# Performance work log

Measured on AMD Instinct MI355X. Metric: run time of the kernel, lower is better.

## Reference

```python
import jax, jax.numpy as jnp
import numpy as np

# ---- module config (matches init_kwargs) ----
TEMPORAL_DIM = 64
INPUT_DIM = 3
NUM_LEVELS = 16
LEVEL_DIM = 2          # C: output channels per level
BASE_RES = 16
LOG2_HASH = 17
DESIRED_RES = 2048
ALIGN_CORNERS = False
PER_LEVEL_SCALE = float(np.exp2(np.log2(DESIRED_RES / BASE_RES) / (NUM_LEVELS - 1)))
S = float(np.log2(PER_LEVEL_SCALE))
GRID_CH = LEVEL_DIM + TEMPORAL_DIM  # channels stored per table row
PRIMES = (1, 2654435761, 805459861)  # InstantNGP fast_hash primes
B = 262144


def _level_params():
    """Static per-level (offset, hashmap_size, resolution, scale) per InstantNGP."""
    params = []
    offset = 0
    max_params = 2 ** LOG2_HASH
    for l in range(NUM_LEVELS):
        scale = float(np.exp2(l * S)) * BASE_RES - 1.0
        resolution = int(np.ceil(scale)) + 1
        res_eff = resolution if ALIGN_CORNERS else resolution + 1
        n = min(max_params, res_eff ** INPUT_DIM)
        n = int(np.ceil(n / 8) * 8)
        params.append((offset, n, resolution, scale))
        offset += n
    return params, offset

LEVELS, TABLE_ROWS = _level_params()


def setup_inputs() -> dict:
    key = jax.random.key(0)
    k1, k2, k3, k4 = jax.random.split(key, 4)
    inputs = jax.random.uniform(k1, (B, INPUT_DIM), dtype=jnp.float32)  # coords in [0,1)
    embeddings = jax.random.uniform(k2, (TABLE_ROWS, GRID_CH), dtype=jnp.float32,
                                    minval=-1e-4, maxval=1e-4)
    # temporal sliding-window rows: per sample/channel, blend two adjacent channels
    idx_a = jax.random.randint(k3, (B, LEVEL_DIM), 0, GRID_CH)
    idx_b = (idx_a + 1) % GRID_CH
    t = jax.random.uniform(k4, (B, LEVEL_DIM), dtype=jnp.float32)
    tri = jnp.stack([1.0 - t, idx_a.astype(jnp.float32), t, idx_b.astype(jnp.float32)],
                    axis=2).reshape(B, 4 * LEVEL_DIM)
    return {"inputs": inputs, "temporal_row_index": tri, "embeddings": embeddings}


def _encode(inputs, temporal_row_index, embeddings):
    n = inputs.shape[0]
    w_a = temporal_row_index[:, 0::4]                       # [B, C]
    idx_a = temporal_row_index[:, 1::4].astype(jnp.int32)   # [B, C]
    w_b = temporal_row_index[:, 2::4]
    idx_b = temporal_row_index[:, 3::4].astype(jnp.int32)
    emb_flat = embeddings.reshape(-1)
    outs = []
    for (offset, hsize, resolution, scale) in LEVELS:
        res_eff = resolution if ALIGN_CORNERS else resolution + 1
        use_hash = (res_eff ** INPUT_DIM) > hsize  # static per level
        pos = inputs * scale + (0.0 if ALIGN_CORNERS else 0.5)  # [B, D]
        pos_floor = jnp.floor(pos)
        frac = pos - pos_floor
        pos_g = pos_floor.astype(jnp.uint32)
        acc = jnp.zeros((n, LEVEL_DIM), embeddings.dtype)
        for corner in range(2 ** INPUT_DIM):
            offs = [(corner >> d) & 1 for d in range(INPUT_DIM)]
            cpos = pos_g + jnp.asarray(offs, dtype=jnp.uint32)  # [B, D]
            w = jnp.ones((n,), inputs.dtype)
            for d in range(INPUT_DIM):
                w = w * (frac[:, d] if offs[d] else 1.0 - frac[:, d])
            if use_hash:
                idx = jnp.zeros((n,), jnp.uint32)
                for d in range(INPUT_DIM):
                    idx = idx ^ (cpos[:, d] * jnp.uint32(PRIMES[d]))  # uint32 wrap
            else:
                idx = jnp.zeros((n,), jnp.uint32)
                stride = 1
                for d in range(INPUT_DIM):
                    idx = idx + cpos[:, d] * jnp.uint32(stride)
                    stride *= res_eff
            row = (idx % jnp.uint32(hsize)).astype(jnp.int32) + offset  # [B]
            base = row[:, None] * GRID_CH
            va = emb_flat[base + idx_a]  # [B, C] temporal channel A
            vb = emb_flat[base + idx_b]  # [B, C] temporal channel B
            acc = acc + w[:, None] * (w_a * va + w_b * vb)
        outs.append(acc)
    # == outputs.permute(1,0,2).reshape(B, L*C)
    return jnp.concatenate(outs, axis=1)


def reference(inputs, temporal_row_index, embeddings):
    return _encode(inputs, temporal_row_index, embeddings)
```

## Files before the change

### kernel.cpp

```cpp
#include <hip/hip_runtime.h>
#include <cmath>

#define NUM_LEVELS 16
#define GRID_CH 66
#define BLOCK 256
#define NGRP 8
#define NSL 14

typedef float float4n __attribute__((ext_vector_type(4)));
typedef float float2n __attribute__((ext_vector_type(2)));

struct LevelP { int offset; int res_eff; int use_hash; int hsize; float scale; };
struct SlP {
    int   offset[NSL];
    int   res_eff[NSL];
    int   use_hash[NSL];
    int   ssz[NSL];
    float scale[NSL];
};

static LevelP g_levels[NUM_LEVELS];
static bool init_levels() {
    long long off = 0;
    const double S = std::log2(2048.0 / 16.0) / 15.0;
    for (int l = 0; l < NUM_LEVELS; ++l) {
        double scale = std::exp2((double)l * S) * 16.0 - 1.0;
        int resolution = (int)std::ceil(scale) + 1;
        int res_eff = resolution + 1;
        long long cube = (long long)res_eff * res_eff * res_eff;
        long long n = cube < 131072 ? cube : 131072;
        n = ((n + 7) / 8) * 8;
        g_levels[l].offset   = (int)off;
        g_levels[l].res_eff  = res_eff;
        g_levels[l].use_hash = (cube > n) ? 1 : 0;
        g_levels[l].hsize    = (int)n;
        g_levels[l].scale    = (float)scale;
        off += n;
    }
    return true;
}
static bool g_inited = init_levels();

struct __attribute__((packed, aligned(4))) F2 { float x, y; };

__global__ __launch_bounds__(BLOCK) void tge_prep(
    const float* __restrict__ inputs, const float* __restrict__ tri,
    float* __restrict__ rec)
{
    const int i = blockIdx.x * BLOCK + threadIdx.x;
    const float4 t0 = *reinterpret_cast<const float4*>(tri + (size_t)i * 8);
    const float4 t1 = *reinterpret_cast<const float4*>(tri + (size_t)i * 8 + 4);
    const unsigned bits = (unsigned)(int)t0.y | ((unsigned)(int)t1.y << 8);
    float4n r0, r1;
    r0.x = inputs[i * 3 + 0]; r0.y = inputs[i * 3 + 1]; r0.z = inputs[i * 3 + 2];
    r0.w = t0.x;
    r1.x = t0.z; r1.y = t1.x; r1.z = t1.z;
    r1.w = __uint_as_float(bits);
    *reinterpret_cast<float4n*>(rec + (size_t)i * 8)     = r0;
    *reinterpret_cast<float4n*>(rec + (size_t)i * 8 + 4) = r1;
}

__global__ __launch_bounds__(BLOCK) void tge_simple(
    const float* __restrict__ rec, const float* __restrict__ tbl,
    float* __restrict__ acc, float scale, int R, int use_hash, int B, int l)
{
    const int i = blockIdx.x * BLOCK + threadIdx.x;
    const float4n r0 = *reinterpret_cast<const float4n*>(rec + (size_t)i * 8);
    const float4n r1 = *reinterpret_cast<const float4n*>(rec + (size_t)i * 8 + 4);
    const unsigned iap = __float_as_uint(r1.w);
    const int  ia0 = (int)(iap & 0xffu), ia1 = (int)((iap >> 8) & 0xffu);
    const unsigned base0 = (unsigned)(ia0 < 64 ? ia0 : 64);
    const unsigned base1 = (unsigned)(ia1 < 64 ? ia1 : 64);
    const bool hi0 = (ia0 == 65), hi1 = (ia1 == 65);

    const float px = r0.x * scale + 0.5f;
    const float py = r0.y * scale + 0.5f;
    const float pz = r0.z * scale + 0.5f;
    const float fx = floorf(px), fy = floorf(py), fz = floorf(pz);
    const float rx = px - fx, ry = py - fy, rz = pz - fz;
    const unsigned ux = (unsigned)fx, uy = (unsigned)fy, uz = (unsigned)fz;

    unsigned hx0, hx1, hy0, hy1, hz0, hz1;
    if (use_hash) {
        hx0 = ux;                   hx1 = ux + 1u;
        hy0 = uy * 2654435761u;     hy1 = hy0 + 2654435761u;
        hz0 = uz * 805459861u;      hz1 = hz0 + 805459861u;
    } else {
        hx0 = ux;                   hx1 = ux + 1u;
        hy0 = uy * (unsigned)R;     hy1 = hy0 + (unsigned)R;
        hz0 = uz * (unsigned)(R*R); hz1 = hz0 + (unsigned)(R*R);
    }

    const float w0x = 1.f - rx, w1x = rx;
    const float w0y = 1.f - ry, w1y = ry;
    const float w0z = 1.f - rz, w1z = rz;

    float acc0 = 0.f, acc1 = 0.f;
    #pragma unroll
    for (int c = 0; c < 8; ++c) {
        const unsigned a = (c & 1) ? hx1 : hx0;
        const unsigned b = (c & 2) ? hy1 : hy0;
        const unsigned d = (c & 4) ? hz1 : hz0;
        const unsigned idx = use_hash ? ((a ^ b ^ d) & 131071u) : (a + b + d);
        const float* rowp = tbl + (size_t)idx * GRID_CH;
        const F2 pa0 = *reinterpret_cast<const F2*>(rowp + base0);
        const F2 pa1 = *reinterpret_cast<const F2*>(rowp + base1);
        const float va0 = hi0 ? pa0.y : pa0.x;
        const float va1 = hi1 ? pa1.y : pa1.x;
        float vb0 = pa0.y, vb1 = pa1.y;
        if (hi0) vb0 = rowp[0];
        if (hi1) vb1 = rowp[0];
        const float wx = (c & 1) ? w1x : w0x;
        const float wy = (c & 2) ? w1y : w0y;
        const float wz = (c & 4) ? w1z : w0z;
        const float w = wx * wy * wz;
        acc0 += w * (r0.w * va0 + r1.x * vb0);
        acc1 += w * (r1.y * va1 + r1.z * vb1);
    }
    float2n rr; rr.x = acc0; rr.y = acc1;
    *reinterpret_cast<float2n*>(acc + ((size_t)l * B + i) * 2) = rr;
}

__global__ __launch_bounds__(BLOCK) void tge_gather(
    const float* __restrict__ rec, const float* __restrict__ emb,
    float* __restrict__ part,
    float* __restrict__ acc,
    SlP P, int B, int ngx)
{
    const int z = blockIdx.z;
    if (blockIdx.x >= ngx) {
        if (z == 0) return;
        const int s = (blockIdx.x - ngx) * BLOCK + threadIdx.x;
        const float* pp = part + (size_t)((z - 1) % 3) * NGRP * B * 2;
        float a0 = 0.f, a1 = 0.f;
        #pragma unroll
        for (int g = 0; g < NGRP; ++g) {
            const float2n v = __builtin_nontemporal_load(
                reinterpret_cast<const float2n*>(pp + ((size_t)g * B + s) * 2));
            a0 += v.x; a1 += v.y;
        }
        float2n r; r.x = a0; r.y = a1;
        *reinterpret_cast<float2n*>(acc + ((size_t)(z + 1) * B + s) * 2) = r;
        return;
    }

    const int g = blockIdx.x & (NGRP - 1);
    const int i = (blockIdx.x >> 3) * BLOCK + threadIdx.x;

    const float4n r0 = *reinterpret_cast<const float4n*>(rec + (size_t)i * 8);
    const float4n r1 = *reinterpret_cast<const float4n*>(rec + (size_t)i * 8 + 4);
    const unsigned iap = __float_as_uint(r1.w);
    const int  ia0 = (int)(iap & 0xffu), ia1 = (int)((iap >> 8) & 0xffu);
    const unsigned base0 = (unsigned)(ia0 < 64 ? ia0 : 64);
    const unsigned base1 = (unsigned)(ia1 < 64 ? ia1 : 64);
    const bool hi0 = (ia0 == 65), hi1 = (ia1 == 65);
    const float wa0 = r0.w, wb0 = r1.x, wa1 = r1.y, wb1 = r1.z;

    const float scale    = P.scale[z];
    const int   R        = P.res_eff[z];
    const int   use_hash = P.use_hash[z];
    const float* __restrict__ tbl = emb + (size_t)P.offset[z] * GRID_CH;

    const float px = r0.x * scale + 0.5f;
    const float py = r0.y * scale + 0.5f;
    const float pz = r0.z * scale + 0.5f;
    const float fx = floorf(px), fy = floorf(py), fz = floorf(pz);
    const float rx = px - fx, ry = py - fy, rz = pz - fz;
    const unsigned ux = (unsigned)fx, uy = (unsigned)fy, uz = (unsigned)fz;

    unsigned hx0, hx1, hy0, hy1, hz0, hz1;
    if (use_hash) {
        hx0 = ux;                   hx1 = ux + 1u;
        hy0 = uy * 2654435761u;     hy1 = hy0 + 2654435761u;
        hz0 = uz * 805459861u;      hz1 = hz0 + 805459861u;
    } else {
        hx0 = ux;                   hx1 = ux + 1u;
        hy0 = uy * (unsigned)R;     hy1 = hy0 + (unsigned)R;
        hz0 = uz * (unsigned)(R*R); hz1 = hz0 + (unsigned)(R*R);
    }

    unsigned w_0, w_1, w_2, w_3, w_4, w_5, w_6, w_7;
    if (use_hash) {
        const unsigned a0 = hy0 ^ hz0, a1 = hy1 ^ hz0;
        const unsigned a2 = hy0 ^ hz1, a3 = hy1 ^ hz1;
        w_0 = (hx0 ^ a0) & 131071u;  w_1 = (hx1 ^ a0) & 131071u;
        w_2 = (hx0 ^ a1) & 131071u;  w_3 = (hx1 ^ a1) & 131071u;
        w_4 = (hx0 ^ a2) & 131071u;  w_5 = (hx1 ^ a2) & 131071u;
        w_6 = (hx0 ^ a3) & 131071u;  w_7 = (hx1 ^ a3) & 131071u;
    } else {
        const unsigned a0 = hy0 + hz0, a1 = hy1 + hz0;
        const unsigned a2 = hy0 + hz1, a3 = hy1 + hz1;
        w_0 = hx0 + a0;  w_1 = hx1 + a0;
        w_2 = hx0 + a1;  w_3 = hx1 + a1;
        w_4 = hx0 + a2;  w_5 = hx1 + a2;
        w_6 = hx0 + a3;  w_7 = hx1 + a3;
    }

    const unsigned lo = (unsigned)(g * P.ssz[z]);
    const unsigned hc = lo + (unsigned)P.ssz[z];
    const bool m0 = (w_0 >= lo) & (w_0 < hc);
    const bool m1 = (w_1 >= lo) & (w_1 < hc);
    const bool m2 = (w_2 >= lo) & (w_2 < hc);
    const bool m3 = (w_3 >= lo) & (w_3 < hc);
    const bool m4 = (w_4 >= lo) & (w_4 < hc);
    const bool m5 = (w_5 >= lo) & (w_5 < hc);
    const bool m6 = (w_6 >= lo) & (w_6 < hc);
    const bool m7 = (w_7 >= lo) & (w_7 < hc);

    const unsigned t0 = w_0 * (unsigned)GRID_CH;
    const unsigned t1 = w_1 * (unsigned)GRID_CH;
    const unsigned t2 = w_2 * (unsigned)GRID_CH;
    const unsigned t3 = w_3 * (unsigned)GRID_CH;
    const unsigned t4 = w_4 * (unsigned)GRID_CH;
    const unsigned t5 = w_5 * (unsigned)GRID_CH;
    const unsigned t6 = w_6 * (unsigned)GRID_CH;
    const unsigned t7 = w_7 * (unsigned)GRID_CH;

    F2 A0{0,0}, A1{0,0}, A2{0,0}, A3{0,0}, A4{0,0}, A5{0,0}, A6{0,0}, A7{0,0};
    F2 B0{0,0}, B1{0,0}, B2{0,0}, B3{0,0}, B4{0,0}, B5{0,0}, B6{0,0}, B7{0,0};
#define LD2(off) (*reinterpret_cast<const F2*>(tbl + (off)))
    if (m0) { A0 = LD2(t0 + base0); B0 = LD2(t0 + base1); }
    if (m1) { A1 = LD2(t1 + base0); B1 = LD2(t1 + base1); }
    if (m2) { A2 = LD2(t2 + base0); B2 = LD2(t2 + base1); }
    if (m3) { A3 = LD2(t3 + base0); B3 = LD2(t3 + base1); }
    if (m4) { A4 = LD2(t4 + base0); B4 = LD2(t4 + base1); }
    if (m5) { A5 = LD2(t5 + base0); B5 = LD2(t5 + base1); }
    if (m6) { A6 = LD2(t6 + base0); B6 = LD2(t6 + base1); }
    if (m7) { A7 = LD2(t7 + base0); B7 = LD2(t7 + base1); }
#undef LD2

    float q00 = A0.y, q01 = A1.y, q02 = A2.y, q03 = A3.y;
    float q04 = A4.y, q05 = A5.y, q06 = A6.y, q07 = A7.y;
    float q10 = B0.y, q11 = B1.y, q12 = B2.y, q13 = B3.y;
    float q14 = B4.y, q15 = B5.y, q16 = B6.y, q17 = B7.y;
    if (hi0) {
        if (m0) q00 = tbl[t0]; if (m1) q01 = tbl[t1];
        if (m2) q02 = tbl[t2]; if (m3) q03 = tbl[t3];
        if (m4) q04 = tbl[t4]; if (m5) q05 = tbl[t5];
        if (m6) q06 = tbl[t6]; if (m7) q07 = tbl[t7];
    }
    if (hi1) {
        if (m0) q10 = tbl[t0]; if (m1) q11 = tbl[t1];
        if (m2) q12 = tbl[t2]; if (m3) q13 = tbl[t3];
        if (m4) q14 = tbl[t4]; if (m5) q15 = tbl[t5];
        if (m6) q16 = tbl[t6]; if (m7) q17 = tbl[t7];
    }

    const float w0x = 1.f - rx, w1x = rx;
    const float w0y = 1.f - ry, w1y = ry;
    const float w0z = 1.f - rz, w1z = rz;

    float acc0 = 0.f, acc1 = 0.f;
#define CACC(A, Bv, q0v, q1v, w)                         \
    { const float va0 = hi0 ? (A).y : (A).x;             \
      const float va1 = hi1 ? (Bv).y : (Bv).x;           \
      acc0 += (w) * (wa0 * va0 + wb0 * (q0v));           \
      acc1 += (w) * (wa1 * va1 + wb1 * (q1v)); }
    CACC(A0, B0, q00, q10, w0x * w0y * w0z)
    CACC(A1, B1, q01, q11, w1x * w0y * w0z)
    CACC(A2, B2, q02, q12, w0x * w1y * w0z)
    CACC(A3, B3, q03, q13, w1x * w1y * w0z)
    CACC(A4, B4, q04, q14, w0x * w0y * w1z)
    CACC(A5, B5, q05, q15, w1x * w0y * w1z)
    CACC(A6, B6, q06, q16, w0x * w1y * w1z)
    CACC(A7, B7, q07, q17, w1x * w1y * w1z)
#undef CACC

    float2n rr; rr.x = acc0; rr.y = acc1;
    __builtin_nontemporal_store(rr, reinterpret_cast<float2n*>(
        part + (((size_t)(z % 3) * NGRP + g) * B + i) * 2));
}

__global__ __launch_bounds__(BLOCK) void tge_reduce_last(
    const float* __restrict__ part, float* __restrict__ acc, int B)
{
    const int s = blockIdx.x * BLOCK + threadIdx.x;
    const float* pp = part + (size_t)(13 % 3) * NGRP * B * 2;
    float a0 = 0.f, a1 = 0.f;
    #pragma unroll
    for (int g = 0; g < NGRP; ++g) {
        const float2n v = __builtin_nontemporal_load(
            reinterpret_cast<const float2n*>(pp + ((size_t)g * B + s) * 2));
        a0 += v.x; a1 += v.y;
    }
    float2n r; r.x = a0; r.y = a1;
    *reinterpret_cast<float2n*>(acc + ((size_t)15 * B + s) * 2) = r;
}

__global__ __launch_bounds__(256) void tge_finish(
    const float* __restrict__ acc, float* __restrict__ out, int B)
{
    __shared__ float tile[64][33];
    const int t  = threadIdx.x;
    const int s  = t & 63;
    const int q  = t >> 6;
    const int gs = blockIdx.x * 64 + s;

    #pragma unroll
    for (int j = 0; j < 4; ++j) {
        const int l = q * 4 + j;
        const float2n v = *reinterpret_cast<const float2n*>(
            acc + ((size_t)l * B + gs) * 2);
        tile[s][2 * l]     = v.x;
        tile[s][2 * l + 1] = v.y;
    }
    __syncthreads();

    #pragma unroll
    for (int k2 = 0; k2 < 2; ++k2) {
        const int gf = t + k2 * 256;
        const int ss = gf >> 3;
        const int c  = (gf & 7) * 4;
        const float4 v = make_float4(tile[ss][c], tile[ss][c + 1],
                                     tile[ss][c + 2], tile[ss][c + 3]);
        *reinterpret_cast<float4*>(out + ((size_t)(blockIdx.x * 64 + ss)) * 32 + c) = v;
    }
}

__global__ __launch_bounds__(BLOCK) void tge_level(
    const float* __restrict__ inputs, const float* __restrict__ tri,
    const float* __restrict__ tbl, float* __restrict__ dst,
    float scale, int R, int use_hash)
{
    const int i = blockIdx.x * BLOCK + threadIdx.x;
    const float x = inputs[i * 3 + 0];
    const float y = inputs[i * 3 + 1];
    const float z = inputs[i * 3 + 2];
    const float4 t0 = *reinterpret_cast<const float4*>(tri + (size_t)i * 8);
    const float4 t1 = *reinterpret_cast<const float4*>(tri + (size_t)i * 8 + 4);
    const int  ia0 = (int)t0.y, ia1 = (int)t1.y;
    const int  base0 = ia0 < 64 ? ia0 : 64;
    const int  base1 = ia1 < 64 ? ia1 : 64;
    const bool hi0 = (ia0 == 65), hi1 = (ia1 == 65);

    const float px = x * scale + 0.5f;
    const float py = y * scale + 0.5f;
    const float pz = z * scale + 0.5f;
    const float fx = floorf(px), fy = floorf(py), fz = floorf(pz);
    const float rx = px - fx, ry = py - fy, rz = pz - fz;
    const unsigned ux = (unsigned)fx, uy = (unsigned)fy, uz = (unsigned)fz;

    unsigned hx0, hx1, hy0, hy1, hz0, hz1;
    if (use_hash) {
        hx0 = ux;                   hx1 = ux + 1u;
        hy0 = uy * 2654435761u;     hy1 = hy0 + 2654435761u;
        hz0 = uz * 805459861u;      hz1 = hz0 + 805459861u;
    } else {
        hx0 = ux;                   hx1 = ux + 1u;
        hy0 = uy * (unsigned)R;     hy1 = hy0 + (unsigned)R;
        hz0 = uz * (unsigned)(R*R); hz1 = hz0 + (unsigned)(R*R);
    }

    const float w0x = 1.f - rx, w1x = rx;
    const float w0y = 1.f - ry, w1y = ry;
    const float w0z = 1.f - rz, w1z = rz;

    float acc0 = 0.f, acc1 = 0.f;
    #pragma unroll
    for (int c = 0; c < 8; ++c) {
        const unsigned a = (c & 1) ? hx1 : hx0;
        const unsigned b = (c & 2) ? hy1 : hy0;
        const unsigned d = (c & 4) ? hz1 : hz0;
        const unsigned idx = use_hash ? ((a ^ b ^ d) & 131071u) : (a + b + d);
        const float* rowp = tbl + (size_t)idx * GRID_CH;
        const F2 pa0 = *reinterpret_cast<const F2*>(rowp + base0);
        const F2 pa1 = *reinterpret_cast<const F2*>(rowp + base1);
        const float va0 = hi0 ? pa0.y : pa0.x;
        const float va1 = hi1 ? pa1.y : pa1.x;
        float vb0 = pa0.y, vb1 = pa1.y;
        if (hi0) vb0 = rowp[0];
        if (hi1) vb1 = rowp[0];
        const float wx = (c & 1) ? w1x : w0x;
        const float wy = (c & 2) ? w1y : w0y;
        const float wz = (c & 4) ? w1z : w0z;
        const float w = wx * wy * wz;
        acc0 += w * (t0.x * va0 + t0.z * vb0);
        acc1 += w * (t1.x * va1 + t1.z * vb1);
    }
    *reinterpret_cast<float2*>(dst + (size_t)i * 32) = make_float2(acc0, acc1);
}

extern "C" void kernel_launch(void* const* d_in, const int* in_sizes, int n_in,
                              void* d_out, int out_size, void* d_ws, size_t ws_size,
                              hipStream_t stream) {
    const float* inputs = (const float*)d_in[0];
    const float* tri    = (const float*)d_in[1];
    const float* emb    = (const float*)d_in[2];
    float* out          = (float*)d_out;

    const int B = in_sizes[0] / 3;

    float* rec  = (float*)d_ws;
    float* acc  = rec + (size_t)B * 8;
    float* part = acc + (size_t)NUM_LEVELS * B * 2;
    const size_t need = ((size_t)B * 8 + (size_t)NUM_LEVELS * B * 2 +
                         (size_t)3 * NGRP * B * 2) * sizeof(float);

    if (ws_size < need) {
        for (int l = 0; l < NUM_LEVELS; ++l) {
            const LevelP& P = g_levels[l];
            tge_level<<<dim3(B / BLOCK), BLOCK, 0, stream>>>(
                inputs, tri, emb + (size_t)P.offset * GRID_CH,
                out + 2 * l, P.scale, P.res_eff, P.use_hash);
        }
        return;
    }

    SlP SP;
    for (int li = 0; li < NSL; ++li) {
        const LevelP& P = g_levels[li + 2];
        SP.offset[li]   = P.offset;
        SP.res_eff[li]  = P.res_eff;
        SP.use_hash[li] = P.use_hash;
        SP.ssz[li]      = P.hsize / NGRP;
        SP.scale[li]    = P.scale;
    }

    tge_prep<<<dim3(B / BLOCK), BLOCK, 0, stream>>>(inputs, tri, rec);

    for (int l = 0; l < 2; ++l) {
        const LevelP& P = g_levels[l];
        tge_simple<<<dim3(B / BLOCK), BLOCK, 0, stream>>>(
            rec, emb + (size_t)P.offset * GRID_CH, acc,
            P.scale, P.res_eff, P.use_hash, B, l);
    }

    const int ngx = NGRP * (B / BLOCK);
    const int nrx = B / BLOCK;
    tge_gather<<<dim3(ngx + nrx, 1, NSL), BLOCK, 0, stream>>>(
        rec, emb, part, acc, SP, B, ngx);

    tge_reduce_last<<<dim3(B / BLOCK), BLOCK, 0, stream>>>(part, acc, B);
    tge_finish<<<dim3(B / 64), 256, 0, stream>>>(acc, out, B);
}
```

Before: 528.9 us.

## Keep all level partials and fold slice reduction into the finish kernel

The gather kernel now writes per-group partials for all 14 hashed levels into separate buffers instead of a 3-deep ring, and each thread handles two sample tiles. The interleaved reduce blocks and the separate last-level reduce kernel are removed, and the finish kernel sums the 8 group partials directly while transposing. This drops one launch and the intermediate accumulator round trip, at the cost of a much larger workspace and more partial traffic that can no longer stay cache-resident in the ring.

```diff
diff --git a/kernel.cpp b/kernel.cpp
--- a/kernel.cpp
+++ b/kernel.cpp
@@ -6,6 +6,7 @@
 #define BLOCK 256
 #define NGRP 8
 #define NSL 14
+#define CHUNK 2
 
 typedef float float4n __attribute__((ext_vector_type(4)));
 typedef float float2n __attribute__((ext_vector_type(2)));
@@ -62,7 +63,7 @@
 
 __global__ __launch_bounds__(BLOCK) void tge_simple(
     const float* __restrict__ rec, const float* __restrict__ tbl,
-    float* __restrict__ acc, float scale, int R, int use_hash, int B, int l)
+    float* __restrict__ acc01, float scale, int R, int use_hash, int B, int l)
 {
     const int i = blockIdx.x * BLOCK + threadIdx.x;
     const float4n r0 = *reinterpret_cast<const float4n*>(rec + (size_t)i * 8);
@@ -118,177 +119,153 @@
         acc1 += w * (r1.y * va1 + r1.z * vb1);
     }
     float2n rr; rr.x = acc0; rr.y = acc1;
-    *reinterpret_cast<float2n*>(acc + ((size_t)l * B + i) * 2) = rr;
+    *reinterpret_cast<float2n*>(acc01 + ((size_t)l * B + i) * 2) = rr;
 }
 
 __global__ __launch_bounds__(BLOCK) void tge_gather(
     const float* __restrict__ rec, const float* __restrict__ emb,
     float* __restrict__ part,
-    float* __restrict__ acc,
-    SlP P, int B, int ngx)
+    SlP P, int B)
 {
-    const int z = blockIdx.z;
-    if (blockIdx.x >= ngx) {
-        if (z == 0) return;
-        const int s = (blockIdx.x - ngx) * BLOCK + threadIdx.x;
-        const float* pp = part + (size_t)((z - 1) % 3) * NGRP * B * 2;
-        float a0 = 0.f, a1 = 0.f;
-        #pragma unroll
-        for (int g = 0; g < NGRP; ++g) {
-            const float2n v = __builtin_nontemporal_load(
-                reinterpret_cast<const float2n*>(pp + ((size_t)g * B + s) * 2));
-            a0 += v.x; a1 += v.y;
-        }
-        float2n r; r.x = a0; r.y = a1;
-        *reinterpret_cast<float2n*>(acc + ((size_t)(z + 1) * B + s) * 2) = r;
-        return;
-    }
-
-    const int g = blockIdx.x & (NGRP - 1);
-    const int i = (blockIdx.x >> 3) * BLOCK + threadIdx.x;
-
-    const float4n r0 = *reinterpret_cast<const float4n*>(rec + (size_t)i * 8);
-    const float4n r1 = *reinterpret_cast<const float4n*>(rec + (size_t)i * 8 + 4);
-    const unsigned iap = __float_as_uint(r1.w);
-    const int  ia0 = (int)(iap & 0xffu), ia1 = (int)((iap >> 8) & 0xffu);
-    const unsigned base0 = (unsigned)(ia0 < 64 ? ia0 : 64);
-    const unsigned base1 = (unsigned)(ia1 < 64 ? ia1 : 64);
-    const bool hi0 = (ia0 == 65), hi1 = (ia1 == 65);
-    const float wa0 = r0.w, wb0 = r1.x, wa1 = r1.y, wb1 = r1.z;
+    const int z  = blockIdx.z;
+    const int g  = blockIdx.x & (NGRP - 1);
+    const int bb = blockIdx.x >> 3;
+    const int tilesPerGrp = (B / BLOCK) / CHUNK;
 
     const float scale    = P.scale[z];
     const int   R        = P.res_eff[z];
     const int   use_hash = P.use_hash[z];
     const float* __restrict__ tbl = emb + (size_t)P.offset[z] * GRID_CH;
-
-    const float px = r0.x * scale + 0.5f;
-    const float py = r0.y * scale + 0.5f;
-    const float pz = r0.z * scale + 0.5f;
-    const float fx = floorf(px), fy = floorf(py), fz = floorf(pz);
-    const float rx = px - fx, ry = py - fy, rz = pz - fz;
-    const unsigned ux = (unsigned)fx, uy = (unsigned)fy, uz = (unsigned)fz;
-
-    unsigned hx0, hx1, hy0, hy1, hz0, hz1;
-    if (use_hash) {
-        hx0 = ux;                   hx1 = ux + 1u;
-        hy0 = uy * 2654435761u;     hy1 = hy0 + 2654435761u;
-        hz0 = uz * 805459861u;      hz1 = hz0 + 805459861u;
-    } else {
-        hx0 = ux;                   hx1 = ux + 1u;
-        hy0 = uy * (unsigned)R;     hy1 = hy0 + (unsigned)R;
-        hz0 = uz * (unsigned)(R*R); hz1 = hz0 + (unsigned)(R*R);
-    }
-
-    unsigned w_0, w_1, w_2, w_3, w_4, w_5, w_6, w_7;
-    if (use_hash) {
-        const unsigned a0 = hy0 ^ hz0, a1 = hy1 ^ hz0;
-        const unsigned a2 = hy0 ^ hz1, a3 = hy1 ^ hz1;
-        w_0 = (hx0 ^ a0) & 131071u;  w_1 = (hx1 ^ a0) & 131071u;
-        w_2 = (hx0 ^ a1) & 131071u;  w_3 = (hx1 ^ a1) & 131071u;
-        w_4 = (hx0 ^ a2) & 131071u;  w_5 = (hx1 ^ a2) & 131071u;
-        w_6 = (hx0 ^ a3) & 131071u;  w_7 = (hx1 ^ a3) & 131071u;
-    } else {
-        const unsigned a0 = hy0 + hz0, a1 = hy1 + hz0;
-        const unsigned a2 = hy0 + hz1, a3 = hy1 + hz1;
-        w_0 = hx0 + a0;  w_1 = hx1 + a0;
-        w_2 = hx0 + a1;  w_3 = hx1 + a1;
-        w_4 = hx0 + a2;  w_5 = hx1 + a2;
-        w_6 = hx0 + a3;  w_7 = hx1 + a3;
-    }
-
     const unsigned lo = (unsigned)(g * P.ssz[z]);
     const unsigned hc = lo + (unsigned)P.ssz[z];
-    const bool m0 = (w_0 >= lo) & (w_0 < hc);
-    const bool m1 = (w_1 >= lo) & (w_1 < hc);
-    const bool m2 = (w_2 >= lo) & (w_2 < hc);
-    const bool m3 = (w_3 >= lo) & (w_3 < hc);
-    const bool m4 = (w_4 >= lo) & (w_4 < hc);
-    const bool m5 = (w_5 >= lo) & (w_5 < hc);
-    const bool m6 = (w_6 >= lo) & (w_6 < hc);
-    const bool m7 = (w_7 >= lo) & (w_7 < hc);
-
-    const unsigned t0 = w_0 * (unsigned)GRID_CH;
-    const unsigned t1 = w_1 * (unsigned)GRID_CH;
-    const unsigned t2 = w_2 * (unsigned)GRID_CH;
-    const unsigned t3 = w_3 * (unsigned)GRID_CH;
-    const unsigned t4 = w_4 * (unsigned)GRID_CH;
-    const unsigned t5 = w_5 * (unsigned)GRID_CH;
-    const unsigned t6 = w_6 * (unsigned)GRID_CH;
-    const unsigned t7 = w_7 * (unsigned)GRID_CH;
-
-    F2 A0{0,0}, A1{0,0}, A2{0,0}, A3{0,0}, A4{0,0}, A5{0,0}, A6{0,0}, A7{0,0};
-    F2 B0{0,0}, B1{0,0}, B2{0,0}, B3{0,0}, B4{0,0}, B5{0,0}, B6{0,0}, B7{0,0};
+    float* __restrict__ pdst = part + (((size_t)z * NGRP + g) * B) * 2;
+
+    #pragma unroll 1
+    for (int c2 = 0; c2 < CHUNK; ++c2) {
+        const int i = (bb + c2 * tilesPerGrp) * BLOCK + threadIdx.x;
+
+        const float4n r0 = *reinterpret_cast<const float4n*>(rec + (size_t)i * 8);
+        const float4n r1 = *reinterpret_cast<const float4n*>(rec + (size_t)i * 8 + 4);
+        const unsigned iap = __float_as_uint(r1.w);
+        const int  ia0 = (int)(iap & 0xffu), ia1 = (int)((iap >> 8) & 0xffu);
+        const unsigned base0 = (unsigned)(ia0 < 64 ? ia0 : 64);
+        const unsigned base1 = (unsigned)(ia1 < 64 ? ia1 : 64);
+        const bool hi0 = (ia0 == 65), hi1 = (ia1 == 65);
+        const float wa0 = r0.w, wb0 = r1.x, wa1 = r1.y, wb1 = r1.z;
+
+        const float px = r0.x * scale + 0.5f;
+        const float py = r0.y * scale + 0.5f;
+        const float pz = r0.z * scale + 0.5f;
+        const float fx = floorf(px), fy = floorf(py), fz = floorf(pz);
+        const float rx = px - fx, ry = py - fy, rz = pz - fz;
+        const unsigned ux = (unsigned)fx, uy = (unsigned)fy, uz = (unsigned)fz;
+
+        unsigned hx0, hx1, hy0, hy1, hz0, hz1;
+        if (use_hash) {
+            hx0 = ux;                   hx1 = ux + 1u;
+            hy0 = uy * 2654435761u;     hy1 = hy0 + 2654435761u;
+            hz0 = uz * 805459861u;      hz1 = hz0 + 805459861u;
+        } else {
+            hx0 = ux;                   hx1 = ux + 1u;
+            hy0 = uy * (unsigned)R;     hy1 = hy0 + (unsigned)R;
+            hz0 = uz * (unsigned)(R*R); hz1 = hz0 + (unsigned)(R*R);
+        }
+
+        unsigned w_0, w_1, w_2, w_3, w_4, w_5, w_6, w_7;
+        if (use_hash) {
+            const unsigned a0 = hy0 ^ hz0, a1 = hy1 ^ hz0;
+            const unsigned a2 = hy0 ^ hz1, a3 = hy1 ^ hz1;
+            w_0 = (hx0 ^ a0) & 131071u;  w_1 = (hx1 ^ a0) & 131071u;
+            w_2 = (hx0 ^ a1) & 131071u;  w_3 = (hx1 ^ a1) & 131071u;
+            w_4 = (hx0 ^ a2) & 131071u;  w_5 = (hx1 ^ a2) & 131071u;
+            w_6 = (hx0 ^ a3) & 131071u;  w_7 = (hx1 ^ a3) & 131071u;
+        } else {
+            const unsigned a0 = hy0 + hz0, a1 = hy1 + hz0;
+            const unsigned a2 = hy0 + hz1, a3 = hy1 + hz1;
+            w_0 = hx0 + a0;  w_1 = hx1 + a0;
+            w_2 = hx0 + a1;  w_3 = hx1 + a1;
+            w_4 = hx0 + a2;  w_5 = hx1 + a2;
+            w_6 = hx0 + a3;  w_7 = hx1 + a3;
+        }
+
+        const bool m0 = (w_0 >= lo) & (w_0 < hc);
+        const bool m1 = (w_1 >= lo) & (w_1 < hc);
+        const bool m2 = (w_2 >= lo) & (w_2 < hc);
+        const bool m3 = (w_3 >= lo) & (w_3 < hc);
+        const bool m4 = (w_4 >= lo) & (w_4 < hc);
+        const bool m5 = (w_5 >= lo) & (w_5 < hc);
+        const bool m6 = (w_6 >= lo) & (w_6 < hc);
+        const bool m7 = (w_7 >= lo) & (w_7 < hc);
+
+        const unsigned t0 = w_0 * (unsigned)GRID_CH;
+        const unsigned t1 = w_1 * (unsigned)GRID_CH;
+        const unsigned t2 = w_2 * (unsigned)GRID_CH;
+        const unsigned t3 = w_3 * (unsigned)GRID_CH;
+        const unsigned t4 = w_4 * (unsigned)GRID_CH;
+        const unsigned t5 = w_5 * (unsigned)GRID_CH;
+        const unsigned t6 = w_6 * (unsigned)GRID_CH;
+        const unsigned t7 = w_7 * (unsigned)GRID_CH;
+
+        F2 A0{0,0}, A1{0,0}, A2{0,0}, A3{0,0}, A4{0,0}, A5{0,0}, A6{0,0}, A7{0,0};
+        F2 B0{0,0}, B1{0,0}, B2{0,0}, B3{0,0}, B4{0,0}, B5{0,0}, B6{0,0}, B7{0,0};
 #define LD2(off) (*reinterpret_cast<const F2*>(tbl + (off)))
-    if (m0) { A0 = LD2(t0 + base0); B0 = LD2(t0 + base1); }
-    if (m1) { A1 = LD2(t1 + base0); B1 = LD2(t1 + base1); }
-    if (m2) { A2 = LD2(t2 + base0); B2 = LD2(t2 + base1); }
-    if (m3) { A3 = LD2(t3 + base0); B3 = LD2(t3 + base1); }
-    if (m4) { A4 = LD2(t4 + base0); B4 = LD2(t4 + base1); }
-    if (m5) { A5 = LD2(t5 + base0); B5 = LD2(t5 + base1); }
-    if (m6) { A6 = LD2(t6 + base0); B6 = LD2(t6 + base1); }
-    if (m7) { A7 = LD2(t7 + base0); B7 = LD2(t7 + base1); }
+        if (m0) { A0 = LD2(t0 + base0); B0 = LD2(t0 + base1); }
+        if (m1) { A1 = LD2(t1 + base0); B1 = LD2(t1 + base1); }
+        if (m2) { A2 = LD2(t2 + base0); B2 = LD2(t2 + base1); }
+        if (m3) { A3 = LD2(t3 + base0); B3 = LD2(t3 + base1); }
+        if (m4) { A4 = LD2(t4 + base0); B4 = LD2(t4 + base1); }
+        if (m5) { A5 = LD2(t5 + base0); B5 = LD2(t5 + base1); }
+        if (m6) { A6 = LD2(t6 + base0); B6 = LD2(t6 + base1); }
+        if (m7) { A7 = LD2(t7 + base0); B7 = LD2(t7 + base1); }
 #undef LD2
 
-    float q00 = A0.y, q01 = A1.y, q02 = A2.y, q03 = A3.y;
-    float q04 = A4.y, q05 = A5.y, q06 = A6.y, q07 = A7.y;
-    float q10 = B0.y, q11 = B1.y, q12 = B2.y, q13 = B3.y;
-    float q14 = B4.y, q15 = B5.y, q16 = B6.y, q17 = B7.y;
-    if (hi0) {
-        if (m0) q00 = tbl[t0]; if (m1) q01 = tbl[t1];
-        if (m2) q02 = tbl[t2]; if (m3) q03 = tbl[t3];
-        if (m4) q04 = tbl[t4]; if (m5) q05 = tbl[t5];
-        if (m6) q06 = tbl[t6]; if (m7) q07 = tbl[t7];
-    }
-    if (hi1) {
-        if (m0) q10 = tbl[t0]; if (m1) q11 = tbl[t1];
-        if (m2) q12 = tbl[t2]; if (m3) q13 = tbl[t3];
-        if (m4) q14 = tbl[t4]; if (m5) q15 = tbl[t5];
-        if (m6) q16 = tbl[t6]; if (m7) q17 = tbl[t7];
-    }
-
-    const float w0x = 1.f - rx, w1x = rx;
-    const float w0y = 1.f - ry, w1y = ry;
-    const float w0z = 1.f - rz, w1z = rz;
-
-    float acc0 = 0.f, acc1 = 0.f;
+        float q00 = A0.y, q01 = A1.y, q02 = A2.y, q03 = A3.y;
+        float q04 = A4.y, q05 = A5.y, q06 = A6.y, q07 = A7.y;
+        float q10 = B0.y, q11 = B1.y, q12 = B2.y, q13 = B3.y;
+        float q14 = B4.y, q15 = B5.y, q16 = B6.y, q17 = B7.y;
+        if (hi0) {
+            if (m0) q00 = tbl[t0]; if (m1) q01 = tbl[t1];
+            if (m2) q02 = tbl[t2]; if (m3) q03 = tbl[t3];
+            if (m4) q04 = tbl[t4]; if (m5) q05 = tbl[t5];
+            if (m6) q06 = tbl[t6]; if (m7) q07 = tbl[t7];
+        }
+        if (hi1) {
+            if (m0) q10 = tbl[t0]; if (m1) q11 = tbl[t1];
+            if (m2) q12 = tbl[t2]; if (m3) q13 = tbl[t3];
+            if (m4) q14 = tbl[t4]; if (m5) q15 = tbl[t5];
+            if (m6) q16 = tbl[t6]; if (m7) q17 = tbl[t7];
+        }
+
+        const float w0x = 1.f - rx, w1x = rx;
+        const float w0y = 1.f - ry, w1y = ry;
+        const float w0z = 1.f - rz, w1z = rz;
+
+        float acc0 = 0.f, acc1 = 0.f;
 #define CACC(A, Bv, q0v, q1v, w)                         \
-    { const float va0 = hi0 ? (A).y : (A).x;             \
-      const float va1 = hi1 ? (Bv).y : (Bv).x;           \
-      acc0 += (w) * (wa0 * va0 + wb0 * (q0v));           \
-      acc1 += (w) * (wa1 * va1 + wb1 * (q1v)); }
-    CACC(A0, B0, q00, q10, w0x * w0y * w0z)
-    CACC(A1, B1, q01, q11, w1x * w0y * w0z)
-    CACC(A2, B2, q02, q12, w0x * w1y * w0z)
-    CACC(A3, B3, q03, q13, w1x * w1y * w0z)
-    CACC(A4, B4, q04, q14, w0x * w0y * w1z)
-    CACC(A5, B5, q05, q15, w1x * w0y * w1z)
-    CACC(A6, B6, q06, q16, w0x * w1y * w1z)
-    CACC(A7, B7, q07, q17, w1x * w1y * w1z)
+        { const float va0 = hi0 ? (A).y : (A).x;         \
+          const float va1 = hi1 ? (Bv).y : (Bv).x;       \
+          acc0 += (w) * (wa0 * va0 + wb0 * (q0v));       \
+          acc1 += (w) * (wa1 * va1 + wb1 * (q1v)); }
+        CACC(A0, B0, q00, q10, w0x * w0y * w0z)
+        CACC(A1, B1, q01, q11, w1x * w0y * w0z)
+        CACC(A2, B2, q02, q12, w0x * w1y * w0z)
+        CACC(A3, B3, q03, q13, w1x * w1y * w0z)
+        CACC(A4, B4, q04, q14, w0x * w0y * w1z)
+        CACC(A5, B5, q05, q15, w1x * w0y * w1z)
+        CACC(A6, B6, q06, q16, w0x * w1y * w1z)
+        CACC(A7, B7, q07, q17, w1x * w1y * w1z)
 #undef CACC
 
-    float2n rr; rr.x = acc0; rr.y = acc1;
-    __builtin_nontemporal_store(rr, reinterpret_cast<float2n*>(
-        part + (((size_t)(z % 3) * NGRP + g) * B + i) * 2));
-}
-
-__global__ __launch_bounds__(BLOCK) void tge_reduce_last(
-    const float* __restrict__ part, float* __restrict__ acc, int B)
-{
-    const int s = blockIdx.x * BLOCK + threadIdx.x;
-    const float* pp = part + (size_t)(13 % 3) * NGRP * B * 2;
-    float a0 = 0.f, a1 = 0.f;
-    #pragma unroll
-    for (int g = 0; g < NGRP; ++g) {
-        const float2n v = __builtin_nontemporal_load(
-            reinterpret_cast<const float2n*>(pp + ((size_t)g * B + s) * 2));
-        a0 += v.x; a1 += v.y;
-    }
-    float2n r; r.x = a0; r.y = a1;
-    *reinterpret_cast<float2n*>(acc + ((size_t)15 * B + s) * 2) = r;
+        float2n rr; rr.x = acc0; rr.y = acc1;
+        __builtin_nontemporal_store(rr,
+            reinterpret_cast<float2n*>(pdst + (size_t)i * 2));
+    }
 }
 
 __global__ __launch_bounds__(256) void tge_finish(
-    const float* __restrict__ acc, float* __restrict__ out, int B)
+    const float* __restrict__ acc01,
+    const float* __restrict__ part,
+    float* __restrict__ out, int B)
 {
     __shared__ float tile[64][33];
     const int t  = threadIdx.x;
@@ -299,10 +276,23 @@
     #pragma unroll
     for (int j = 0; j < 4; ++j) {
         const int l = q * 4 + j;
-        const float2n v = *reinterpret_cast<const float2n*>(
-            acc + ((size_t)l * B + gs) * 2);
-        tile[s][2 * l]     = v.x;
-        tile[s][2 * l + 1] = v.y;
+        float a0, a1;
+        if (l < 2) {
+            const float2n v = *reinterpret_cast<const float2n*>(
+                acc01 + ((size_t)l * B + gs) * 2);
+            a0 = v.x; a1 = v.y;
+        } else {
+            a0 = 0.f; a1 = 0.f;
+            const float* p = part + ((size_t)(l - 2) * NGRP * B + gs) * 2;
+            #pragma unroll
+            for (int g = 0; g < NGRP; ++g) {
+                const float2n v = __builtin_nontemporal_load(
+                    reinterpret_cast<const float2n*>(p + (size_t)g * B * 2));
+                a0 += v.x; a1 += v.y;
+            }
+        }
+        tile[s][2 * l]     = a0;
+        tile[s][2 * l + 1] = a1;
     }
     __syncthreads();
 
@@ -390,11 +380,11 @@
 
     const int B = in_sizes[0] / 3;
 
-    float* rec  = (float*)d_ws;
-    float* acc  = rec + (size_t)B * 8;
-    float* part = acc + (size_t)NUM_LEVELS * B * 2;
-    const size_t need = ((size_t)B * 8 + (size_t)NUM_LEVELS * B * 2 +
-                         (size_t)3 * NGRP * B * 2) * sizeof(float);
+    float* rec   = (float*)d_ws;
+    float* acc01 = rec + (size_t)B * 8;
+    float* part  = acc01 + (size_t)2 * B * 2;
+    const size_t need = ((size_t)B * 8 + (size_t)2 * B * 2 +
+                         (size_t)NSL * NGRP * B * 2) * sizeof(float);
 
     if (ws_size < need) {
         for (int l = 0; l < NUM_LEVELS; ++l) {
@@ -421,15 +411,12 @@
     for (int l = 0; l < 2; ++l) {
         const LevelP& P = g_levels[l];
         tge_simple<<<dim3(B / BLOCK), BLOCK, 0, stream>>>(
-            rec, emb + (size_t)P.offset * GRID_CH, acc,
+            rec, emb + (size_t)P.offset * GRID_CH, acc01,
             P.scale, P.res_eff, P.use_hash, B, l);
     }
 
-    const int ngx = NGRP * (B / BLOCK);
-    const int nrx = B / BLOCK;
-    tge_gather<<<dim3(ngx + nrx, 1, NSL), BLOCK, 0, stream>>>(
-        rec, emb, part, acc, SP, B, ngx);
-
-    tge_reduce_last<<<dim3(B / BLOCK), BLOCK, 0, stream>>>(part, acc, B);
-    tge_finish<<<dim3(B / 64), 256, 0, stream>>>(acc, out, B);
-}
+    const int ngx = NGRP * ((B / BLOCK) / CHUNK);
+    tge_gather<<<dim3(ngx, 1, NSL), BLOCK, 0, stream>>>(rec, emb, part, SP, B);
+
+    tge_finish<<<dim3(B / 64), 256, 0, stream>>>(acc01, part, out, B);
+}
```

New measurement: 571.3 us. +8.0%, slower.
